# Optimization experiments

Measured on AMD Instinct MI355X. Metric: run time of the kernel, lower is better.

Reference implementation:

```python
import jax, jax.numpy as jnp
import numpy as np

SCALE_DIM = 64  # output_size, used as 1/sqrt(d) scale per source code


def setup_inputs() -> dict:
    key = jax.random.key(0)
    ks = jax.random.split(key, 6)
    B, S, D_IN, D_OUT = 4, 4096, 512, 64
    return {
        "key_inputs": jax.random.normal(ks[0], (B, S, D_IN), dtype=jnp.float32),
        "value_inputs": jax.random.normal(ks[1], (B, S, D_IN), dtype=jnp.float32),
        "query_inputs": jax.random.normal(ks[2], (B, S, D_IN), dtype=jnp.float32),
        "Wq": jax.random.normal(ks[3], (D_IN, D_OUT), dtype=jnp.float32) * 0.05,
        "Wk": jax.random.normal(ks[4], (D_IN, D_OUT), dtype=jnp.float32) * 0.05,
        "Wv": jax.random.normal(ks[5], (D_IN, D_OUT), dtype=jnp.float32) * 0.05,
    }


def reference(key_inputs, value_inputs, query_inputs, Wq, Wk, Wv):
    # QKV projections: [B,S,D_in] x [D_in,D_out] -> [B,S,D_out]
    Q = jnp.einsum("bsd,de->bse", query_inputs, Wq)
    K = jnp.einsum("bsd,de->bse", key_inputs, Wk)
    V = jnp.einsum("bsd,de->bse", value_inputs, Wv)
    d = K.shape[2]
    # scores: [B, Sq, Sk]
    scores = jnp.einsum("bqe,bke->bqk", Q, K) / jnp.sqrt(jnp.float32(d))
    # causal mask: strictly-upper-triangular -inf (source: transpose(tril(-inf, -1)))
    Sq, Sk = Q.shape[1], K.shape[1]
    causal = jnp.tril(jnp.ones((Sq, Sk), dtype=bool))
    scores = jnp.where(causal[None, :, :], scores, -jnp.inf)
    attn = jax.nn.softmax(scores, axis=-1)
    Z = jnp.einsum("bqk,bke->bqe", attn, V)
    return Z
```

## Files before the change

kernel.cpp:

```cpp
#include <hip/hip_runtime.h>
#include <hip/hip_bf16.h>

#define BATCH 4
#define SEQ   4096
#define DIN   512
#define DOUT  64

typedef __attribute__((ext_vector_type(4))) float f32x4;
typedef __attribute__((ext_vector_type(8))) short bf16x8;
typedef __attribute__((ext_vector_type(4))) short bf16x4;

__device__ __forceinline__ f32x4 mfma16(bf16x8 a, bf16x8 b, f32x4 c) {
    return __builtin_amdgcn_mfma_f32_16x16x32_bf16(a, b, c, 0, 0, 0);
}
__device__ __forceinline__ f32x4 mfma16k(bf16x4 a, bf16x4 b, f32x4 c) {
    return __builtin_amdgcn_mfma_f32_16x16x16bf16_1k(a, b, c, 0, 0, 0);
}

__device__ __forceinline__ short f2bf(float f) {
    union { float f; unsigned u; } x; x.f = f;
    unsigned r = x.u + 0x7FFFu + ((x.u >> 16) & 1u);
    return (short)(r >> 16);
}

__device__ __forceinline__ unsigned pack_bf2(float lo, float hi) {
    union { float f; unsigned u; } a, b; a.f = lo; b.f = hi;
    return __builtin_amdgcn_perm(b.u, a.u, 0x07060302u);
}

__device__ __forceinline__ void dma16(const void* g, void* l) {
    __builtin_amdgcn_global_load_lds(
        (const __attribute__((address_space(1))) void*)g,
        (__attribute__((address_space(3))) void*)l, 16, 0, 0);
}

#define QSCALE 0.1803368801111204f

__global__ __launch_bounds__(256) void wconv_kernel(
    const float* __restrict__ Wq, const float* __restrict__ Wk,
    const float* __restrict__ Wv, short* __restrict__ Wt)
{
    const int m = blockIdx.y;
    const float* W = (m == 0) ? Wq : (m == 1) ? Wk : Wv;
    const int idx = blockIdx.x * 256 + threadIdx.x;
    const int k = idx >> 6;
    const int n = idx & 63;
    Wt[m * (DOUT * DIN) + n * DIN + k] = f2bf(W[idx]);
}

__global__ __launch_bounds__(256) void proj_kernel(
    const float* __restrict__ Xq, const float* __restrict__ Xk, const float* __restrict__ Xv,
    const short* __restrict__ Wt,
    short* __restrict__ Qb, short* __restrict__ Kb, short* __restrict__ Vt)
{
    __shared__ __align__(16) char smem[2][24576];

    const int m = blockIdx.y;
    const float* X  = (m == 0) ? Xq : (m == 1) ? Xk : Xv;
    const short* Wm = Wt + m * (DOUT * DIN);

    const int tid  = threadIdx.x;
    const int wv   = tid >> 6;
    const int lane = tid & 63;
    const int quad = lane >> 4;
    const int l16  = lane & 15;
    const long waveRow = (long)blockIdx.x * 64 + wv * 16;

    const float* xg = X  + (waveRow + l16) * DIN + quad * 8;
    const short* wg = Wm + (long)(wv * 16 + l16) * DIN + quad * 8;

    f32x4 acc[4];
    #pragma unroll
    for (int e = 0; e < 4; ++e) acc[e] = (f32x4){0.f, 0.f, 0.f, 0.f};

#define STAGE_PROJ(B) do {                                   \
        char* xb_ = &smem[(B)][0] + wv * 4096;               \
        char* wb_ = &smem[(B)][0] + 16384 + wv * 2048;       \
        dma16(xg,      xb_);                                 \
        dma16(xg + 4,  xb_ + 1024);                          \
        dma16(xg + 32, xb_ + 2048);                          \
        dma16(xg + 36, xb_ + 3072);                          \
        dma16(wg,      wb_);                                 \
        dma16(wg + 32, wb_ + 1024);                          \
    } while (0)

    STAGE_PROJ(0);
    xg += 64; wg += 64;
    __syncthreads();

    for (int kt = 0; kt < 8; ++kt) {
        const int cur = kt & 1;
        if (kt < 7) {
            if (cur) { STAGE_PROJ(0); } else { STAGE_PROJ(1); }
            xg += 64; wg += 64;
        }
        const char* xb = &smem[cur][0] + wv * 4096;
        const char* wb = &smem[cur][0] + 16384;
        #pragma unroll
        for (int c2 = 0; c2 < 2; ++c2) {
            float4 xa = *(const float4*)(xb + c2 * 2048 + lane * 16);
            float4 xc = *(const float4*)(xb + c2 * 2048 + 1024 + lane * 16);
            bf16x8 af;
            af[0] = f2bf(xa.x); af[1] = f2bf(xa.y); af[2] = f2bf(xa.z); af[3] = f2bf(xa.w);
            af[4] = f2bf(xc.x); af[5] = f2bf(xc.y); af[6] = f2bf(xc.z); af[7] = f2bf(xc.w);
            #pragma unroll
            for (int e = 0; e < 4; ++e) {
                bf16x8 bf = *(const bf16x8*)(wb + (e * 2 + c2) * 1024 + lane * 16);
                if (m < 2) acc[e] = mfma16(af, bf, acc[e]);
                else       acc[e] = mfma16(bf, af, acc[e]);
            }
        }
        __syncthreads();
    }
#undef STAGE_PROJ

    if (m < 2) {
        short* O = (m == 0) ? Qb : Kb;
        const float sc = (m == 0) ? QSCALE : 1.0f;
        #pragma unroll
        for (int e = 0; e < 4; ++e)
            #pragma unroll
            for (int r = 0; r < 4; ++r)
                O[(waveRow + quad * 4 + r) * DOUT + e * 16 + l16] = f2bf(acc[e][r] * sc);
    } else {
        const long b = waveRow >> 12;
        const long s = waveRow & (SEQ - 1);
        #pragma unroll
        for (int e = 0; e < 4; ++e)
            #pragma unroll
            for (int r = 0; r < 4; ++r)
                Vt[(b * DOUT + e * 16 + quad * 4 + r) * SEQ + s + l16] = f2bf(acc[e][r]);
    }
}

__global__ __launch_bounds__(256) void flash_kernel(
    const short* __restrict__ Qb, const short* __restrict__ Kb,
    const short* __restrict__ Vt, float* __restrict__ Out)
{
    __shared__ __align__(16) char smem[2][32768];

    const int i    = blockIdx.x;
    const int b    = (i & 7) >> 1;
    const int t    = 127 - (((i >> 3) << 1) | (i & 1));
    const int tid  = threadIdx.x;
    const int wv   = tid >> 6;
    const int lane = tid & 63;
    const int quad = lane >> 4;
    const int l16  = lane & 15;
    const int wq   = wv >> 1;
    const int wk   = wv & 1;
    const int q0w  = t * 32 + wq * 16;

    const short* Qp = Qb + ((long)b * SEQ + q0w + l16) * DOUT + quad * 8;
    bf16x8 qf0 = *(const bf16x8*)(Qp);
    bf16x8 qf1 = *(const bf16x8*)(Qp + 32);

    const short* Kbase  = Kb + (long)b * SEQ * DOUT;
    const short* VbaseG = Vt + (long)b * DOUT * SEQ;

    const short* gk = Kbase + (long)(wv * 16 + l16) * DOUT + quad * 8;
    const int erow = 4 * wv + (lane >> 4);
    const int cgr  = (lane & 15) ^ (erow & 15);
    const short* gv = VbaseG + (long)erow * SEQ + cgr * 8;

    f32x4 acc[4];
    #pragma unroll
    for (int e = 0; e < 4; ++e) acc[e] = (f32x4){0.f, 0.f, 0.f, 0.f};
    float mrow = -1e30f, lrow = 0.f;

    const int q_hi   = q0w + 15;
    const int qg     = q0w + l16;
    const int wfirst = wk * 64;
    const int R      = t / 4 + 1;

#define STAGE_KV(B, KV0) do {                                         \
        char* kb_ = &smem[(B)][0];                                    \
        char* vb_ = &smem[(B)][0] + 16384;                            \
        const short* gkp_ = gk + (long)(KV0) * DOUT;                  \
        dma16(gkp_,                  kb_ + (2 * wv) * 1024);          \
        dma16(gkp_ + 32,             kb_ + (2 * wv + 1) * 1024);      \
        dma16(gkp_ + 64 * DOUT,      kb_ + (2 * wv + 8) * 1024);      \
        dma16(gkp_ + 64 * DOUT + 32, kb_ + (2 * wv + 9) * 1024);      \
        const short* gvp_ = gv + (KV0);                               \
        dma16(gvp_,            vb_ + (wv)      * 1024);               \
        dma16(gvp_ + 16 * SEQ, vb_ + (wv + 4)  * 1024);               \
        dma16(gvp_ + 32 * SEQ, vb_ + (wv + 8)  * 1024);               \
        dma16(gvp_ + 48 * SEQ, vb_ + (wv + 12) * 1024);               \
    } while (0)

    STAGE_KV(0, 0);
    __syncthreads();

    for (int r = 0; r < R; ++r) {
        const int kv0 = r * 128;
        const int cur = r & 1;
        if (r + 1 < R) STAGE_KV(cur ^ 1, kv0 + 128);

        if ((kv0 + wfirst) <= q_hi) {
            const char* kb = &smem[cur][0];
            const char* vb = &smem[cur][0] + 16384;

            f32x4 sc[4];
            #pragma unroll
            for (int kh = 0; kh < 4; ++kh) {
                const int slot = (wk * 4 + kh) * 2;
                bf16x8 k0 = *(const bf16x8*)(kb + slot * 1024 + lane * 16);
                bf16x8 k1 = *(const bf16x8*)(kb + (slot + 1) * 1024 + lane * 16);
                f32x4 z = (f32x4){0.f, 0.f, 0.f, 0.f};
                z = mfma16(k0, qf0, z);
                z = mfma16(k1, qf1, z);
                sc[kh] = z;
            }

            #pragma unroll
            for (int kh = 0; kh < 4; ++kh)
                #pragma unroll
                for (int rr = 0; rr < 4; ++rr)
                    sc[kh][rr] = ((kv0 + wfirst + kh * 16 + quad * 4 + rr) <= qg)
                               ? sc[kh][rr] : -1e30f;

            float tm = -1e30f;
            #pragma unroll
            for (int kh = 0; kh < 4; ++kh)
                #pragma unroll
                for (int rr = 0; rr < 4; ++rr) tm = fmaxf(tm, sc[kh][rr]);
            tm = fmaxf(tm, __shfl_xor(tm, 16, 64));
            tm = fmaxf(tm, __shfl_xor(tm, 32, 64));
            const float mn = fmaxf(mrow, tm);
            const float alpha = __builtin_amdgcn_exp2f(mrow - mn);
            mrow = mn;
            float p[4][4];
            float rs = 0.f;
            #pragma unroll
            for (int kh = 0; kh < 4; ++kh)
                #pragma unroll
                for (int rr = 0; rr < 4; ++rr) {
                    p[kh][rr] = __builtin_amdgcn_exp2f(sc[kh][rr] - mn);
                    rs += p[kh][rr];
                }
            rs += __shfl_xor(rs, 16, 64);
            rs += __shfl_xor(rs, 32, 64);
            lrow = lrow * alpha + rs;
            #pragma unroll
            for (int e = 0; e < 4; ++e)
                #pragma unroll
                for (int rr = 0; rr < 4; ++rr) acc[e][rr] *= alpha;

            union { unsigned u[2]; bf16x4 v; } pf[4];
            #pragma unroll
            for (int kh = 0; kh < 4; ++kh) {
                pf[kh].u[0] = pack_bf2(p[kh][0], p[kh][1]);
                pf[kh].u[1] = pack_bf2(p[kh][2], p[kh][3]);
            }

            #pragma unroll
            for (int kh = 0; kh < 4; ++kh) {
                const int gbase = wk * 8 + kh * 2 + (quad >> 1);
                #pragma unroll
                for (int et = 0; et < 4; ++et) {
                    const int e = et * 16 + l16;
                    bf16x4 cv = *(const bf16x4*)(vb + e * 256
                                   + ((gbase ^ (e & 15)) * 16) + (quad & 1) * 8);
                    acc[et] = mfma16k(cv, pf[kh].v, acc[et]);
                }
            }
        }
        __syncthreads();
    }
#undef STAGE_KV

    float* s_m   = (float*)&smem[0][0];
    float* s_l   = s_m + 64;
    float* s_acc = s_l + 64;

    if (quad == 0) { s_m[wv * 16 + l16] = mrow; s_l[wv * 16 + l16] = lrow; }
    #pragma unroll
    for (int et = 0; et < 4; ++et)
        #pragma unroll
        for (int rr = 0; rr < 4; ++rr)
            s_acc[(wv * 16 + l16) * 65 + et * 16 + quad * 4 + rr] = acc[et][rr];
    __syncthreads();

    const int col   = tid & 63;
    const int rbase = (tid >> 6) * 8;
    float* outp = Out + ((long)b * SEQ + t * 32) * DOUT;
    #pragma unroll
    for (int k = 0; k < 8; ++k) {
        const int row = rbase + k;
        const int w0  = (row >> 4) * 2;
        const int lr  = row & 15;
        const float m0 = s_m[w0 * 16 + lr], m1 = s_m[(w0 + 1) * 16 + lr];
        const float mM = fmaxf(m0, m1);
        const float a0 = __builtin_amdgcn_exp2f(m0 - mM);
        const float a1 = __builtin_amdgcn_exp2f(m1 - mM);
        const float li = a0 * s_l[w0 * 16 + lr] + a1 * s_l[(w0 + 1) * 16 + lr];
        const float o  = a0 * s_acc[(w0 * 16 + lr) * 65 + col]
                       + a1 * s_acc[((w0 + 1) * 16 + lr) * 65 + col];
        outp[row * DOUT + col] = o / li;
    }
}

extern "C" void kernel_launch(void* const* d_in, const int* in_sizes, int n_in,
                              void* d_out, int out_size, void* d_ws, size_t ws_size,
                              hipStream_t stream) {
    const float* key_in   = (const float*)d_in[0];
    const float* value_in = (const float*)d_in[1];
    const float* query_in = (const float*)d_in[2];
    const float* Wq = (const float*)d_in[3];
    const float* Wk = (const float*)d_in[4];
    const float* Wv = (const float*)d_in[5];
    float* out = (float*)d_out;

    short* Qb = (short*)d_ws;
    short* Kb = Qb + (long)BATCH * SEQ * DOUT;
    short* Vt = Kb + (long)BATCH * SEQ * DOUT;
    short* Wt = Vt + (long)BATCH * SEQ * DOUT;

    dim3 wgrid((DOUT * DIN) / 256, 3);
    wconv_kernel<<<wgrid, 256, 0, stream>>>(Wq, Wk, Wv, Wt);

    dim3 pgrid(BATCH * SEQ / 64, 3);
    proj_kernel<<<pgrid, 256, 0, stream>>>(query_in, key_in, value_in,
                                           Wt, Qb, Kb, Vt);

    flash_kernel<<<dim3(SEQ / 32 * BATCH), 256, 0, stream>>>(Qb, Kb, Vt, out);
}
```

Before: 181.8 us.

## Use 8 waves per block splitting KV tile four ways, skip redundant masking and rescale

Raises the flash kernel to 512 threads, so each 16-query row group is split across four waves that each handle 32 keys of the 128-key tile instead of two waves handling 64. Each wave now loads less K/V per stage, and the final merge combines four partial softmax states. It also skips the causal mask on tiles that lie fully below the diagonal, and skips the accumulator rescale when no lane's row max grows. The block-to-tile mapping changes so the second half of blocks runs in ascending order. This adds more parallelism per block and cuts per-wave work, at the cost of more shared-memory merge work and register or occupancy pressure.

```diff
diff --git a/kernel.cpp b/kernel.cpp
--- a/kernel.cpp
+++ b/kernel.cpp
@@ -133,7 +133,7 @@
     }
 }
 
-__global__ __launch_bounds__(256) void flash_kernel(
+__global__ __launch_bounds__(512, 4) void flash_kernel(
     const short* __restrict__ Qb, const short* __restrict__ Kb,
     const short* __restrict__ Vt, float* __restrict__ Out)
 {
@@ -141,14 +141,17 @@
 
     const int i    = blockIdx.x;
     const int b    = (i & 7) >> 1;
-    const int t    = 127 - (((i >> 3) << 1) | (i & 1));
+    const int half = i >> 8;
+    const int v    = (((i >> 3) & 31) << 1) | (i & 1);
+    const int t    = half ? v : (127 - v);
+
     const int tid  = threadIdx.x;
     const int wv   = tid >> 6;
     const int lane = tid & 63;
     const int quad = lane >> 4;
     const int l16  = lane & 15;
-    const int wq   = wv >> 1;
-    const int wk   = wv & 1;
+    const int wq   = wv >> 2;
+    const int wk   = wv & 3;
     const int q0w  = t * 32 + wq * 16;
 
     const short* Qp = Qb + ((long)b * SEQ + q0w + l16) * DOUT + quad * 8;
@@ -159,8 +162,8 @@
     const short* VbaseG = Vt + (long)b * DOUT * SEQ;
 
     const short* gk = Kbase + (long)(wv * 16 + l16) * DOUT + quad * 8;
-    const int erow = 4 * wv + (lane >> 4);
-    const int cgr  = (lane & 15) ^ (erow & 15);
+    const int erow = 4 * wv + quad;
+    const int cgr  = l16 ^ (erow & 15);
     const short* gv = VbaseG + (long)erow * SEQ + cgr * 8;
 
     f32x4 acc[4];
@@ -170,22 +173,18 @@
 
     const int q_hi   = q0w + 15;
     const int qg     = q0w + l16;
-    const int wfirst = wk * 64;
+    const int wfirst = wk * 32;
     const int R      = t / 4 + 1;
 
 #define STAGE_KV(B, KV0) do {                                         \
         char* kb_ = &smem[(B)][0];                                    \
         char* vb_ = &smem[(B)][0] + 16384;                            \
         const short* gkp_ = gk + (long)(KV0) * DOUT;                  \
-        dma16(gkp_,                  kb_ + (2 * wv) * 1024);          \
-        dma16(gkp_ + 32,             kb_ + (2 * wv + 1) * 1024);      \
-        dma16(gkp_ + 64 * DOUT,      kb_ + (2 * wv + 8) * 1024);      \
-        dma16(gkp_ + 64 * DOUT + 32, kb_ + (2 * wv + 9) * 1024);      \
+        dma16(gkp_,      kb_ + (2 * wv) * 1024);                      \
+        dma16(gkp_ + 32, kb_ + (2 * wv + 1) * 1024);                  \
         const short* gvp_ = gv + (KV0);                               \
-        dma16(gvp_,            vb_ + (wv)      * 1024);               \
-        dma16(gvp_ + 16 * SEQ, vb_ + (wv + 4)  * 1024);               \
-        dma16(gvp_ + 32 * SEQ, vb_ + (wv + 8)  * 1024);               \
-        dma16(gvp_ + 48 * SEQ, vb_ + (wv + 12) * 1024);               \
+        dma16(gvp_,            vb_ + (wv)     * 1024);                \
+        dma16(gvp_ + 32 * SEQ, vb_ + (wv + 8) * 1024);                \
     } while (0)
 
     STAGE_KV(0, 0);
@@ -200,10 +199,10 @@
             const char* kb = &smem[cur][0];
             const char* vb = &smem[cur][0] + 16384;
 
-            f32x4 sc[4];
-            #pragma unroll
-            for (int kh = 0; kh < 4; ++kh) {
-                const int slot = (wk * 4 + kh) * 2;
+            f32x4 sc[2];
+            #pragma unroll
+            for (int kh = 0; kh < 2; ++kh) {
+                const int slot = (wk * 2 + kh) * 2;
                 bf16x8 k0 = *(const bf16x8*)(kb + slot * 1024 + lane * 16);
                 bf16x8 k1 = *(const bf16x8*)(kb + (slot + 1) * 1024 + lane * 16);
                 f32x4 z = (f32x4){0.f, 0.f, 0.f, 0.f};
@@ -212,50 +211,53 @@
                 sc[kh] = z;
             }
 
-            #pragma unroll
-            for (int kh = 0; kh < 4; ++kh)
+            if (kv0 + wfirst + 31 > q0w) {
                 #pragma unroll
-                for (int rr = 0; rr < 4; ++rr)
-                    sc[kh][rr] = ((kv0 + wfirst + kh * 16 + quad * 4 + rr) <= qg)
-                               ? sc[kh][rr] : -1e30f;
-
-            float tm = -1e30f;
-            #pragma unroll
-            for (int kh = 0; kh < 4; ++kh)
-                #pragma unroll
-                for (int rr = 0; rr < 4; ++rr) tm = fmaxf(tm, sc[kh][rr]);
+                for (int kh = 0; kh < 2; ++kh)
+                    #pragma unroll
+                    for (int rr = 0; rr < 4; ++rr)
+                        sc[kh][rr] = ((kv0 + wfirst + kh * 16 + quad * 4 + rr) <= qg)
+                                   ? sc[kh][rr] : -1e30f;
+            }
+
+            float tm = fmaxf(fmaxf(fmaxf(sc[0][0], sc[0][1]), fmaxf(sc[0][2], sc[0][3])),
+                             fmaxf(fmaxf(sc[1][0], sc[1][1]), fmaxf(sc[1][2], sc[1][3])));
             tm = fmaxf(tm, __shfl_xor(tm, 16, 64));
             tm = fmaxf(tm, __shfl_xor(tm, 32, 64));
-            const float mn = fmaxf(mrow, tm);
-            const float alpha = __builtin_amdgcn_exp2f(mrow - mn);
-            mrow = mn;
-            float p[4][4];
-            float rs = 0.f;
-            #pragma unroll
-            for (int kh = 0; kh < 4; ++kh)
+            if (!__all(tm <= mrow)) {
+                const float mn = fmaxf(mrow, tm);
+                const float alpha = __builtin_amdgcn_exp2f(mrow - mn);
+                mrow = mn;
+                lrow *= alpha;
+                #pragma unroll
+                for (int e = 0; e < 4; ++e)
+                    #pragma unroll
+                    for (int rr = 0; rr < 4; ++rr) acc[e][rr] *= alpha;
+            }
+            float p[2][4];
+            float rs0 = 0.f, rs1 = 0.f;
+            #pragma unroll
+            for (int kh = 0; kh < 2; ++kh)
                 #pragma unroll
                 for (int rr = 0; rr < 4; ++rr) {
-                    p[kh][rr] = __builtin_amdgcn_exp2f(sc[kh][rr] - mn);
-                    rs += p[kh][rr];
+                    p[kh][rr] = __builtin_amdgcn_exp2f(sc[kh][rr] - mrow);
+                    if (kh == 0) rs0 += p[kh][rr]; else rs1 += p[kh][rr];
                 }
+            float rs = rs0 + rs1;
             rs += __shfl_xor(rs, 16, 64);
             rs += __shfl_xor(rs, 32, 64);
-            lrow = lrow * alpha + rs;
-            #pragma unroll
-            for (int e = 0; e < 4; ++e)
-                #pragma unroll
-                for (int rr = 0; rr < 4; ++rr) acc[e][rr] *= alpha;
-
-            union { unsigned u[2]; bf16x4 v; } pf[4];
-            #pragma unroll
-            for (int kh = 0; kh < 4; ++kh) {
+            lrow += rs;
+
+            union { unsigned u[2]; bf16x4 v; } pf[2];
+            #pragma unroll
+            for (int kh = 0; kh < 2; ++kh) {
                 pf[kh].u[0] = pack_bf2(p[kh][0], p[kh][1]);
                 pf[kh].u[1] = pack_bf2(p[kh][2], p[kh][3]);
             }
 
             #pragma unroll
-            for (int kh = 0; kh < 4; ++kh) {
-                const int gbase = wk * 8 + kh * 2 + (quad >> 1);
+            for (int kh = 0; kh < 2; ++kh) {
+                const int gbase = wk * 4 + kh * 2 + (quad >> 1);
                 #pragma unroll
                 for (int et = 0; et < 4; ++et) {
                     const int e = et * 16 + l16;
@@ -270,8 +272,8 @@
 #undef STAGE_KV
 
     float* s_m   = (float*)&smem[0][0];
-    float* s_l   = s_m + 64;
-    float* s_acc = s_l + 64;
+    float* s_l   = s_m + 128;
+    float* s_acc = s_l + 128;
 
     if (quad == 0) { s_m[wv * 16 + l16] = mrow; s_l[wv * 16 + l16] = lrow; }
     #pragma unroll
@@ -282,20 +284,28 @@
     __syncthreads();
 
     const int col   = tid & 63;
-    const int rbase = (tid >> 6) * 8;
+    const int rbase = (tid >> 6) * 4;
     float* outp = Out + ((long)b * SEQ + t * 32) * DOUT;
     #pragma unroll
-    for (int k = 0; k < 8; ++k) {
+    for (int k = 0; k < 4; ++k) {
         const int row = rbase + k;
-        const int w0  = (row >> 4) * 2;
+        const int w0  = (row >> 4) * 4;
         const int lr  = row & 15;
-        const float m0 = s_m[w0 * 16 + lr], m1 = s_m[(w0 + 1) * 16 + lr];
-        const float mM = fmaxf(m0, m1);
+        const float m0 = s_m[(w0 + 0) * 16 + lr];
+        const float m1 = s_m[(w0 + 1) * 16 + lr];
+        const float m2 = s_m[(w0 + 2) * 16 + lr];
+        const float m3 = s_m[(w0 + 3) * 16 + lr];
+        const float mM = fmaxf(fmaxf(m0, m1), fmaxf(m2, m3));
         const float a0 = __builtin_amdgcn_exp2f(m0 - mM);
         const float a1 = __builtin_amdgcn_exp2f(m1 - mM);
-        const float li = a0 * s_l[w0 * 16 + lr] + a1 * s_l[(w0 + 1) * 16 + lr];
-        const float o  = a0 * s_acc[(w0 * 16 + lr) * 65 + col]
-                       + a1 * s_acc[((w0 + 1) * 16 + lr) * 65 + col];
+        const float a2 = __builtin_amdgcn_exp2f(m2 - mM);
+        const float a3 = __builtin_amdgcn_exp2f(m3 - mM);
+        const float li = a0 * s_l[(w0 + 0) * 16 + lr] + a1 * s_l[(w0 + 1) * 16 + lr]
+                       + a2 * s_l[(w0 + 2) * 16 + lr] + a3 * s_l[(w0 + 3) * 16 + lr];
+        const float o  = a0 * s_acc[((w0 + 0) * 16 + lr) * 65 + col]
+                       + a1 * s_acc[((w0 + 1) * 16 + lr) * 65 + col]
+                       + a2 * s_acc[((w0 + 2) * 16 + lr) * 65 + col]
+                       + a3 * s_acc[((w0 + 3) * 16 + lr) * 65 + col];
         outp[row * DOUT + col] = o / li;
     }
 }
@@ -323,5 +333,5 @@
     proj_kernel<<<pgrid, 256, 0, stream>>>(query_in, key_in, value_in,
                                            Wt, Qb, Kb, Vt);
 
-    flash_kernel<<<dim3(SEQ / 32 * BATCH), 256, 0, stream>>>(Qb, Kb, Vt, out);
-}
+    flash_kernel<<<dim3(SEQ / 32 * BATCH), 512, 0, stream>>>(Qb, Kb, Vt, out);
+}
```

New measurement: 170.3 us. 6.3% less time.
